# Optimization experiments

Measured on AMD Instinct MI355X. Metric: run time of the kernel, lower is better.

Reference implementation:

```python
import jax, jax.numpy as jnp
import numpy as np

B, N, H, D, MAXH, MRP = 64, 197, 12, 64, 16, 14  # batch, tokens (14x14+cls), heads, head_dim, supernet max heads, max rel pos
TABLE = 2 * MRP + 2  # 30 rows per table


def setup_inputs() -> dict:
    key = jax.random.key(0)
    ks = jax.random.split(key, 5)
    x = jax.random.normal(ks[0], (B, N, 3 * D * MAXH), dtype=jnp.float32)
    mk = lambda k: (0.02 * jax.random.normal(k, (TABLE, D), dtype=jnp.float32))
    return {"x": x, "tk_v": mk(ks[1]), "tk_h": mk(ks[2]), "tv_v": mk(ks[3]), "tv_h": mk(ks[4])}


def _rel_pos_emb(table_v, table_h, n):
    # RelativePosition2D_super.forward(length_q=n, length_k=n)
    lq = n - 1
    s = int(np.sqrt(lq))  # 14
    r = jnp.arange(lq)
    dv = r[None, :] // s - r[:, None] // s
    dh = r[None, :] % s - r[:, None] % s
    iv = jnp.clip(dv, -MRP, MRP) + MRP + 1
    ih = jnp.clip(dh, -MRP, MRP) + MRP + 1
    iv = jnp.pad(iv, ((1, 0), (1, 0)))  # CLS row/col -> index 0
    ih = jnp.pad(ih, ((1, 0), (1, 0)))
    return table_v[iv] + table_h[ih]  # (n, n, D)


def reference(x, tk_v, tk_h, tv_v, tv_h):
    scale = D ** (-0.5)  # sample_scale = 64**-0.5
    xs = x[:, :, : H * D * 3]
    qkv = xs.reshape(B, N, 3, H, D).transpose(2, 0, 3, 1, 4)  # (3,B,H,N,D)
    q, k, v = qkv[0], qkv[1], qkv[2]
    attn = jnp.einsum('bhid,bhjd->bhij', q, k) * scale
    rk = _rel_pos_emb(tk_v, tk_h, N)  # (N,N,D)
    attn = attn + jnp.einsum('bhid,ijd->bhij', q, rk) * scale
    attn = jax.nn.softmax(attn, axis=-1)  # attn_drop p=0.0 -> identity
    out = jnp.einsum('bhij,bhjd->bhid', attn, v)
    rv = _rel_pos_emb(tv_v, tv_h, N)  # (N,N,D)
    out = out + jnp.einsum('bhij,ijd->bhid', attn, rv)
    out = out.transpose(0, 2, 1, 3).reshape(B, N, H * D)  # (B,N,768)
    return jnp.pad(out, ((0, 0), (0, 0), (0, MAXH * D - H * D)))  # pad to (B,N,1024)
```

## Files before the change

kernel.cpp:

```cpp
#include <hip/hip_runtime.h>

typedef float  f4v   __attribute__((ext_vector_type(4)));
typedef float  f32x4 __attribute__((ext_vector_type(4)));
typedef short  s8v   __attribute__((ext_vector_type(8)));
typedef short  s4v   __attribute__((ext_vector_type(4)));
typedef __bf16 bf16x8 __attribute__((ext_vector_type(8)));

#define N_   197
#define H_   12
#define CIN  3072
#define COUT 1024
#define VSTR 296
#define ASTR 72
#define BSTR 40
#define G_INDV 8960
#define G_INDH 12544
#define TABSZ  16128

#define MEMBAR() asm volatile("" ::: "memory")

__device__ __forceinline__ unsigned short f2bf(float f) {
    unsigned u = __float_as_uint(f);
    u += 0x7FFFu + ((u >> 16) & 1u);
    return (unsigned short)(u >> 16);
}
__device__ __forceinline__ f32x4 mfma_bf16(s8v a, s8v b, f32x4 c) {
    return __builtin_amdgcn_mfma_f32_16x16x32_bf16(
        __builtin_bit_cast(bf16x8, a), __builtin_bit_cast(bf16x8, b), c, 0, 0, 0);
}
__device__ __forceinline__ void st4f(volatile unsigned short* p, float a, float b, float c, float d) {
    s4v v;
    v[0] = (short)f2bf(a); v[1] = (short)f2bf(b);
    v[2] = (short)f2bf(c); v[3] = (short)f2bf(d);
    *(volatile s4v*)p = v;
}
__device__ __forceinline__ void st4z(volatile unsigned short* p) {
    s4v v = {0, 0, 0, 0};
    *(volatile s4v*)p = v;
}

__global__ void init_tabs(unsigned short* __restrict__ g) {
    int idx = blockIdx.x * 256 + threadIdx.x;
    if (idx >= TABSZ) return;
    unsigned short v = 0;
    if (idx < G_INDV) {
        int k = idx / 40, c = idx - k * 40;
        if (c < 32) {
            if (k >= 1 && k <= 196) {
                int mj = (k - 1) / 14, cj = (k - 1) - mj * 14;
                if (c == mj || c == 16 + cj) v = (unsigned short)0x3F80;
            } else if (k == 0) {
                if (c == 15 || c == 31) v = (unsigned short)0x3F80;
            }
        }
    } else {
        int t = idx - G_INDV;
        int tab = t / 3584;
        int r = t - tab * 3584;
        int m = r / 224, k = r - m * 224;
        if (k >= 1 && k <= 196) {
            int km1 = k - 1;
            int mk = tab ? (km1 % 14) : (km1 / 14);
            if (mk == m) v = (unsigned short)0x3F80;
        }
    }
    g[idx] = v;
}

__launch_bounds__(1024, 4)
__global__ void attn_super(const float* __restrict__ x,
                           const float* __restrict__ tkv,
                           const float* __restrict__ tkh,
                           const float* __restrict__ tvv,
                           const float* __restrict__ tvh,
                           const unsigned short* __restrict__ gt,
                           float* __restrict__ out) {
    __shared__ __align__(16) unsigned short Kl[272 * 72];
    __shared__ __align__(16) unsigned short Vt[64 * VSTR];
    __shared__ __align__(16) unsigned short AR[16][16 * ASTR];
    __shared__ __align__(16) unsigned short TAB[TABSZ];

    const unsigned short* Bext = TAB;
    const unsigned short* INDv = TAB + G_INDV;
    const unsigned short* INDh = TAB + G_INDH;

    const int bid = blockIdx.x;
    const int b = bid / H_, h = bid % H_;
    const int tid = threadIdx.x;
    const int w  = tid >> 6;
    const int l  = tid & 63;
    const int lg = l >> 4;
    const int ln = l & 15;

    const float* xb = x + (size_t)b * N_ * CIN;

    if (h < 4) {
        float* oz = out + (size_t)b * N_ * COUT + 768 + h * 64;
        for (int idx = tid; idx < N_ * 16; idx += 1024) {
            int row = idx >> 4, c4 = idx & 15;
            f4v z = {0.f, 0.f, 0.f, 0.f};
            *(f4v*)(oz + (size_t)row * COUT + c4 * 4) = z;
        }
    }

    f4v kr[5];
    #pragma unroll
    for (int it = 0; it < 5; ++it) {
        int idx = it * 1024 + tid;
        bool a5 = (it < 4) || (tid < 256);
        int row = idx >> 4, d0 = (idx & 15) * 4;
        f4v v = {0.f, 0.f, 0.f, 0.f};
        if (a5) {
            if (row < N_)                     v = *(const f4v*)(xb + (size_t)row * CIN + 768 + h * 64 + d0);
            else if (row >= 208 && row < 238) v = *(const f4v*)(tkv + (row - 208) * 64 + d0);
            else if (row >= 240 && row < 270) v = *(const f4v*)(tkh + (row - 240) * 64 + d0);
        }
        kr[it] = v;
    }
    f4v q1[2], q2[2];
    if (w < 13) {
        int qrow = w * 16 + ln; if (qrow > 196) qrow = 196;
        const float* qp = xb + (size_t)qrow * CIN + h * 64;
        #pragma unroll
        for (int s2 = 0; s2 < 2; ++s2) {
            q1[s2] = *(const f4v*)(qp + s2 * 32 + lg * 8);
            q2[s2] = *(const f4v*)(qp + s2 * 32 + lg * 8 + 4);
        }
    }
    f4v vr[5];
    #pragma unroll
    for (int it = 0; it < 5; ++it) {
        int idx = it * 1024 + tid;
        bool a5 = (it < 4) || (tid < 512);
        int j = idx % 288, d0 = (idx / 288) * 4;
        f4v v = {0.f, 0.f, 0.f, 0.f};
        if (a5) {
            if (j < N_)                     v = *(const f4v*)(xb + (size_t)j * CIN + 1536 + h * 64 + d0);
            else if (j >= 224 && j < 254)   v = *(const f4v*)(tvv + (j - 224) * 64 + d0);
            else if (j >= 256 && j < 286)   v = *(const f4v*)(tvh + (j - 256) * 64 + d0);
        }
        vr[it] = v;
    }
    for (int idx = tid; idx < TABSZ / 8; idx += 1024) {
        const s8v tv = *(const s8v*)(&gt[idx * 8]);
        *(s8v*)(&TAB[idx * 8]) = tv;
    }

    #pragma unroll
    for (int it = 0; it < 5; ++it) {
        int idx = it * 1024 + tid;
        bool a5 = (it < 4) || (tid < 256);
        if (a5) {
            int row = idx >> 4, d0 = (idx & 15) * 4;
            f4v v = kr[it];
            s4v pk;
            pk[0] = (short)f2bf(v[0]); pk[1] = (short)f2bf(v[1]);
            pk[2] = (short)f2bf(v[2]); pk[3] = (short)f2bf(v[3]);
            *(s4v*)(&Kl[row * 72 + d0]) = pk;
        }
    }
    __syncthreads();

    const int tile = w, qb = tile * 16;
    const unsigned short* ar = &AR[w][0];
    volatile unsigned short* arv = &AR[w][0];

    f32x4 S[13];
    float rsq[4], p0q[4];
    int ritq[4], citq[4];
    if (w < 13) {
        const int iL  = qb + ln;
        const int im1 = (iL > 0) ? iL - 1 : 0;
        const int rit = im1 / 14;
        const int cit = im1 - rit * 14;

        s8v aq[2];
        #pragma unroll
        for (int s2 = 0; s2 < 2; ++s2) {
            #pragma unroll
            for (int e = 0; e < 4; ++e) {
                aq[s2][e]     = (short)f2bf(q1[s2][e] * 0.125f);
                aq[s2][e + 4] = (short)f2bf(q2[s2][e] * 0.125f);
            }
        }
        float spv = 0.f, sph = 0.f;
        #pragma unroll
        for (int tt = 0; tt < 4; ++tt) {
            f32x4 acc = {0.f, 0.f, 0.f, 0.f};
            #pragma unroll
            for (int s2 = 0; s2 < 2; ++s2) {
                const s8v bk = *(const s8v*)(&Kl[((13 + tt) * 16 + ln) * 72 + s2 * 32 + lg * 8]);
                acc = mfma_bf16(bk, aq[s2], acc);
            }
            const bool isV  = (tt < 2);
            const int mbase = (tt & 1) * 16;
            const int shift = isV ? rit : cit;
            const int cbase = isV ? 0 : 16;
            const bool skip0 = (tile == 0 && ln == 0);
            #pragma unroll
            for (int r = 0; r < 4; ++r) {
                int m = mbase + 4 * lg + r;
                int t = m + shift - 15;
                if (!skip0 && m < 30 && t >= 0 && t < 15)
                    arv[ln * ASTR + cbase + t] = f2bf(acc[r]);
                if (!skip0 && m == 0)
                    arv[ln * ASTR + cbase + 15] = f2bf(acc[r]);
            }
            if (tile == 0 && l == 0) {
                if (tt == 0) spv = acc[0];
                if (tt == 2) sph = acc[0];
            }
        }
        if (tile == 0 && l == 0) {
            unsigned short v0 = f2bf(spv), h0 = f2bf(sph);
            #pragma unroll
            for (int t = 0; t < 16; ++t) {
                arv[t] = v0;
                arv[16 + t] = h0;
            }
        }
        MEMBAR();
        const s8v aq2 = *(const s8v*)(&ar[ln * ASTR + lg * 8]);
        __builtin_amdgcn_s_setprio(1);
        #pragma unroll
        for (int ct = 0; ct < 13; ++ct) {
            const s8v be = *(const s8v*)(&Bext[(ct * 16 + ln) * BSTR + lg * 8]);
            f32x4 acc = {0.f, 0.f, 0.f, 0.f};
            acc = mfma_bf16(be, aq2, acc);
            #pragma unroll
            for (int s2 = 0; s2 < 2; ++s2) {
                const s8v bk = *(const s8v*)(&Kl[(ct * 16 + ln) * 72 + s2 * 32 + lg * 8]);
                acc = mfma_bf16(bk, aq[s2], acc);
            }
            S[ct] = acc;
        }
        __builtin_amdgcn_s_setprio(0);
    }
    #pragma unroll
    for (int it = 0; it < 5; ++it) {
        int idx = it * 1024 + tid;
        bool a5 = (it < 4) || (tid < 512);
        if (a5) {
            int j = idx % 288, d0 = (idx / 288) * 4;
            f4v v = vr[it];
            #pragma unroll
            for (int e = 0; e < 4; ++e)
                Vt[(d0 + e) * VSTR + j] = f2bf(v[e]);
        }
    }

    if (w < 13) {
        float rs4[4] = {0.f, 0.f, 0.f, 0.f};
        #pragma unroll
        for (int ct = 0; ct < 13; ++ct) {
            #pragma unroll
            for (int r = 0; r < 4; ++r) {
                float p = __expf(S[ct][r]);
                if (ct == 12) { if (4 * lg + r > 4) p = 0.f; }
                S[ct][r] = p;
                rs4[r] += p;
            }
        }
        float rs = (rs4[0] + rs4[1]) + (rs4[2] + rs4[3]);
        rs += __shfl_xor(rs, 16);
        rs += __shfl_xor(rs, 32);
        float p00 = S[0][0];
        #pragma unroll
        for (int r = 0; r < 4; ++r) {
            rsq[r] = __shfl(rs,  4 * lg + r);
            p0q[r] = __shfl(p00, 4 * lg + r);
        }
        #pragma unroll
        for (int r = 0; r < 4; ++r) {
            int qr2 = qb + 4 * lg + r;
            int im  = (qr2 > 0) ? qr2 - 1 : 0;
            ritq[r] = im / 14;
            citq[r] = im - ritq[r] * 14;
        }
    }
    __syncthreads();

    if (w >= 13) return;

    f32x4 oacc[4];
    #pragma unroll
    for (int nt = 0; nt < 4; ++nt) { f32x4 z = {0.f,0.f,0.f,0.f}; oacc[nt] = z; }
    f32x4 cwv = {0.f,0.f,0.f,0.f}, cwh = {0.f,0.f,0.f,0.f};

    __builtin_amdgcn_s_setprio(1);
    #pragma unroll
    for (int win = 0; win < 3; ++win) {
        MEMBAR();
        #pragma unroll
        for (int cc = 0; cc < 4; ++cc) {
            int ct = win * 4 + cc;
            st4f(&arv[ln * ASTR + cc * 16 + 4 * lg], S[ct][0], S[ct][1], S[ct][2], S[ct][3]);
        }
        MEMBAR();
        #pragma unroll
        for (int kk = 0; kk < 2; ++kk) {
            int kt = win * 2 + kk;
            const s8v ap = *(const s8v*)(&ar[ln * ASTR + kk * 32 + lg * 8]);
            #pragma unroll
            for (int nt = 0; nt < 4; ++nt) {
                const s8v bv = *(const s8v*)(&Vt[(nt * 16 + ln) * VSTR + kt * 32 + lg * 8]);
                oacc[nt] = mfma_bf16(ap, bv, oacc[nt]);
            }
            const s8v bi = *(const s8v*)(&INDv[ln * 224 + kt * 32 + lg * 8]);
            cwv = mfma_bf16(ap, bi, cwv);
            const s8v bh = *(const s8v*)(&INDh[ln * 224 + kt * 32 + lg * 8]);
            cwh = mfma_bf16(ap, bh, cwh);
        }
    }
    {
        MEMBAR();
        st4f(&arv[ln * ASTR + 4 * lg], S[12][0], S[12][1], S[12][2], S[12][3]);
        st4z(&arv[ln * ASTR + 16 + 4 * lg]);
        st4z(&arv[ln * ASTR + 32 + lg * 8]);
        st4z(&arv[ln * ASTR + 36 + lg * 8]);
        MEMBAR();
        {
            const s8v ap = *(const s8v*)(&ar[ln * ASTR + lg * 8]);
            #pragma unroll
            for (int nt = 0; nt < 4; ++nt) {
                const s8v bv = *(const s8v*)(&Vt[(nt * 16 + ln) * VSTR + 192 + lg * 8]);
                oacc[nt] = mfma_bf16(ap, bv, oacc[nt]);
            }
            const s8v bi = *(const s8v*)(&INDv[ln * 224 + 192 + lg * 8]);
            cwv = mfma_bf16(ap, bi, cwv);
            const s8v bh = *(const s8v*)(&INDh[ln * 224 + 192 + lg * 8]);
            cwh = mfma_bf16(ap, bh, cwh);
        }
        MEMBAR();
        #pragma unroll
        for (int r = 0; r < 4; ++r) {
            int q = 4 * lg + r;
            bool isRow0 = (tile == 0) && (q == 0);
            if (ln <= 13 && !isRow0)
                arv[q * ASTR + 47 + ln - ritq[r]] = f2bf(cwv[r]);
            if (ln == 15)
                arv[q * ASTR + 32] = f2bf(isRow0 ? rsq[r] : p0q[r]);
        }
        MEMBAR();
        {
            const s8v ap = *(const s8v*)(&ar[ln * ASTR + 32 + lg * 8]);
            #pragma unroll
            for (int nt = 0; nt < 4; ++nt) {
                const s8v bv = *(const s8v*)(&Vt[(nt * 16 + ln) * VSTR + 224 + lg * 8]);
                oacc[nt] = mfma_bf16(ap, bv, oacc[nt]);
            }
        }
    }
    {
        MEMBAR();
        st4z(&arv[ln * ASTR + lg * 8]);
        st4z(&arv[ln * ASTR + 4 + lg * 8]);
        MEMBAR();
        #pragma unroll
        for (int r = 0; r < 4; ++r) {
            int q = 4 * lg + r;
            bool isRow0 = (tile == 0) && (q == 0);
            if (ln <= 13 && !isRow0)
                arv[q * ASTR + 15 + ln - citq[r]] = f2bf(cwh[r]);
            if (ln == 15)
                arv[q * ASTR + 0] = f2bf(isRow0 ? rsq[r] : p0q[r]);
        }
        MEMBAR();
        {
            const s8v ap = *(const s8v*)(&ar[ln * ASTR + lg * 8]);
            #pragma unroll
            for (int nt = 0; nt < 4; ++nt) {
                const s8v bv = *(const s8v*)(&Vt[(nt * 16 + ln) * VSTR + 256 + lg * 8]);
                oacc[nt] = mfma_bf16(ap, bv, oacc[nt]);
            }
        }
    }
    __builtin_amdgcn_s_setprio(0);
    #pragma unroll
    for (int r = 0; r < 4; ++r) {
        int n = qb + 4 * lg + r;
        if (n < N_) {
            float sc = 1.0f / rsq[r];
            float* orow = out + ((size_t)b * N_ + n) * COUT + h * 64;
            #pragma unroll
            for (int nt = 0; nt < 4; ++nt)
                orow[nt * 16 + ln] = oacc[nt][r] * sc;
        }
    }
}

extern "C" void kernel_launch(void* const* d_in, const int* in_sizes, int n_in,
                              void* d_out, int out_size, void* d_ws, size_t ws_size,
                              hipStream_t stream) {
    const float* x   = (const float*)d_in[0];
    const float* tkv = (const float*)d_in[1];
    const float* tkh = (const float*)d_in[2];
    const float* tvv = (const float*)d_in[3];
    const float* tvh = (const float*)d_in[4];
    float* o = (float*)d_out;
    unsigned short* gt = (unsigned short*)d_ws;
    init_tabs<<<dim3(63), dim3(256), 0, stream>>>(gt);
    attn_super<<<dim3(64 * H_), dim3(1024), 0, stream>>>(x, tkv, tkh, tvv, tvh, gt, o);
}
```

Baseline: 74.73 us.

## Alias K and V LDS buffers and read constant tables from global memory

```diff
diff --git a/kernel.cpp b/kernel.cpp
--- a/kernel.cpp
+++ b/kernel.cpp
@@ -18,6 +18,12 @@
 #define TABSZ  16128
 
 #define MEMBAR() asm volatile("" ::: "memory")
+
+__device__ __forceinline__ void barrier_lds() {
+    asm volatile("s_waitcnt lgkmcnt(0)" ::: "memory");
+    __builtin_amdgcn_s_barrier();
+    asm volatile("" ::: "memory");
+}
 
 __device__ __forceinline__ unsigned short f2bf(float f) {
     unsigned u = __float_as_uint(f);
@@ -67,7 +73,7 @@
     g[idx] = v;
 }
 
-__launch_bounds__(1024, 4)
+__launch_bounds__(1024, 8)
 __global__ void attn_super(const float* __restrict__ x,
                            const float* __restrict__ tkv,
                            const float* __restrict__ tkh,
@@ -75,14 +81,8 @@
                            const float* __restrict__ tvh,
                            const unsigned short* __restrict__ gt,
                            float* __restrict__ out) {
-    __shared__ __align__(16) unsigned short Kl[272 * 72];
-    __shared__ __align__(16) unsigned short Vt[64 * VSTR];
+    __shared__ __align__(16) unsigned short KV[272 * 72];
     __shared__ __align__(16) unsigned short AR[16][16 * ASTR];
-    __shared__ __align__(16) unsigned short TAB[TABSZ];
-
-    const unsigned short* Bext = TAB;
-    const unsigned short* INDv = TAB + G_INDV;
-    const unsigned short* INDh = TAB + G_INDH;
 
     const int bid = blockIdx.x;
     const int b = bid / H_, h = bid % H_;
@@ -141,10 +141,6 @@
         }
         vr[it] = v;
     }
-    for (int idx = tid; idx < TABSZ / 8; idx += 1024) {
-        const s8v tv = *(const s8v*)(&gt[idx * 8]);
-        *(s8v*)(&TAB[idx * 8]) = tv;
-    }
 
     #pragma unroll
     for (int it = 0; it < 5; ++it) {
@@ -156,18 +152,16 @@
             s4v pk;
             pk[0] = (short)f2bf(v[0]); pk[1] = (short)f2bf(v[1]);
             pk[2] = (short)f2bf(v[2]); pk[3] = (short)f2bf(v[3]);
-            *(s4v*)(&Kl[row * 72 + d0]) = pk;
-        }
-    }
-    __syncthreads();
+            *(s4v*)(&KV[row * 72 + d0]) = pk;
+        }
+    }
+    barrier_lds();
 
     const int tile = w, qb = tile * 16;
     const unsigned short* ar = &AR[w][0];
     volatile unsigned short* arv = &AR[w][0];
 
     f32x4 S[13];
-    float rsq[4], p0q[4];
-    int ritq[4], citq[4];
     if (w < 13) {
         const int iL  = qb + ln;
         const int im1 = (iL > 0) ? iL - 1 : 0;
@@ -189,7 +183,7 @@
             f32x4 acc = {0.f, 0.f, 0.f, 0.f};
             #pragma unroll
             for (int s2 = 0; s2 < 2; ++s2) {
-                const s8v bk = *(const s8v*)(&Kl[((13 + tt) * 16 + ln) * 72 + s2 * 32 + lg * 8]);
+                const s8v bk = *(const s8v*)(&KV[((13 + tt) * 16 + ln) * 72 + s2 * 32 + lg * 8]);
                 acc = mfma_bf16(bk, aq[s2], acc);
             }
             const bool isV  = (tt < 2);
@@ -221,21 +215,21 @@
         }
         MEMBAR();
         const s8v aq2 = *(const s8v*)(&ar[ln * ASTR + lg * 8]);
-        __builtin_amdgcn_s_setprio(1);
         #pragma unroll
         for (int ct = 0; ct < 13; ++ct) {
-            const s8v be = *(const s8v*)(&Bext[(ct * 16 + ln) * BSTR + lg * 8]);
+            const s8v be = *(const s8v*)(&gt[(ct * 16 + ln) * BSTR + lg * 8]);
             f32x4 acc = {0.f, 0.f, 0.f, 0.f};
             acc = mfma_bf16(be, aq2, acc);
             #pragma unroll
             for (int s2 = 0; s2 < 2; ++s2) {
-                const s8v bk = *(const s8v*)(&Kl[(ct * 16 + ln) * 72 + s2 * 32 + lg * 8]);
+                const s8v bk = *(const s8v*)(&KV[(ct * 16 + ln) * 72 + s2 * 32 + lg * 8]);
                 acc = mfma_bf16(bk, aq[s2], acc);
             }
             S[ct] = acc;
         }
-        __builtin_amdgcn_s_setprio(0);
-    }
+    }
+    barrier_lds();
+
     #pragma unroll
     for (int it = 0; it < 5; ++it) {
         int idx = it * 1024 + tid;
@@ -245,10 +239,12 @@
             f4v v = vr[it];
             #pragma unroll
             for (int e = 0; e < 4; ++e)
-                Vt[(d0 + e) * VSTR + j] = f2bf(v[e]);
-        }
-    }
-
+                KV[(d0 + e) * VSTR + j] = f2bf(v[e]);
+        }
+    }
+
+    float rsq[4], p0q[4];
+    int ritq[4], citq[4];
     if (w < 13) {
         float rs4[4] = {0.f, 0.f, 0.f, 0.f};
         #pragma unroll
@@ -278,7 +274,7 @@
             citq[r] = im - ritq[r] * 14;
         }
     }
-    __syncthreads();
+    barrier_lds();
 
     if (w >= 13) return;
 
@@ -287,7 +283,6 @@
     for (int nt = 0; nt < 4; ++nt) { f32x4 z = {0.f,0.f,0.f,0.f}; oacc[nt] = z; }
     f32x4 cwv = {0.f,0.f,0.f,0.f}, cwh = {0.f,0.f,0.f,0.f};
 
-    __builtin_amdgcn_s_setprio(1);
     #pragma unroll
     for (int win = 0; win < 3; ++win) {
         MEMBAR();
@@ -303,12 +298,12 @@
             const s8v ap = *(const s8v*)(&ar[ln * ASTR + kk * 32 + lg * 8]);
             #pragma unroll
             for (int nt = 0; nt < 4; ++nt) {
-                const s8v bv = *(const s8v*)(&Vt[(nt * 16 + ln) * VSTR + kt * 32 + lg * 8]);
+                const s8v bv = *(const s8v*)(&KV[(nt * 16 + ln) * VSTR + kt * 32 + lg * 8]);
                 oacc[nt] = mfma_bf16(ap, bv, oacc[nt]);
             }
-            const s8v bi = *(const s8v*)(&INDv[ln * 224 + kt * 32 + lg * 8]);
+            const s8v bi = *(const s8v*)(&gt[G_INDV + ln * 224 + kt * 32 + lg * 8]);
             cwv = mfma_bf16(ap, bi, cwv);
-            const s8v bh = *(const s8v*)(&INDh[ln * 224 + kt * 32 + lg * 8]);
+            const s8v bh = *(const s8v*)(&gt[G_INDH + ln * 224 + kt * 32 + lg * 8]);
             cwh = mfma_bf16(ap, bh, cwh);
         }
     }
@@ -323,12 +318,12 @@
             const s8v ap = *(const s8v*)(&ar[ln * ASTR + lg * 8]);
             #pragma unroll
             for (int nt = 0; nt < 4; ++nt) {
-                const s8v bv = *(const s8v*)(&Vt[(nt * 16 + ln) * VSTR + 192 + lg * 8]);
+                const s8v bv = *(const s8v*)(&KV[(nt * 16 + ln) * VSTR + 192 + lg * 8]);
                 oacc[nt] = mfma_bf16(ap, bv, oacc[nt]);
             }
-            const s8v bi = *(const s8v*)(&INDv[ln * 224 + 192 + lg * 8]);
+            const s8v bi = *(const s8v*)(&gt[G_INDV + ln * 224 + 192 + lg * 8]);
             cwv = mfma_bf16(ap, bi, cwv);
-            const s8v bh = *(const s8v*)(&INDh[ln * 224 + 192 + lg * 8]);
+            const s8v bh = *(const s8v*)(&gt[G_INDH + ln * 224 + 192 + lg * 8]);
             cwh = mfma_bf16(ap, bh, cwh);
         }
         MEMBAR();
@@ -346,7 +341,7 @@
             const s8v ap = *(const s8v*)(&ar[ln * ASTR + 32 + lg * 8]);
             #pragma unroll
             for (int nt = 0; nt < 4; ++nt) {
-                const s8v bv = *(const s8v*)(&Vt[(nt * 16 + ln) * VSTR + 224 + lg * 8]);
+                const s8v bv = *(const s8v*)(&KV[(nt * 16 + ln) * VSTR + 224 + lg * 8]);
                 oacc[nt] = mfma_bf16(ap, bv, oacc[nt]);
             }
         }
@@ -370,12 +365,11 @@
             const s8v ap = *(const s8v*)(&ar[ln * ASTR + lg * 8]);
             #pragma unroll
             for (int nt = 0; nt < 4; ++nt) {
-                const s8v bv = *(const s8v*)(&Vt[(nt * 16 + ln) * VSTR + 256 + lg * 8]);
+                const s8v bv = *(const s8v*)(&KV[(nt * 16 + ln) * VSTR + 256 + lg * 8]);
                 oacc[nt] = mfma_bf16(ap, bv, oacc[nt]);
             }
         }
     }
-    __builtin_amdgcn_s_setprio(0);
     #pragma unroll
     for (int r = 0; r < 4; ++r) {
         int n = qb + 4 * lg + r;
```

Result: slower. 190.9 us (+155.4%).
